# Optimization experiments

Measured on AMD Instinct MI355X. Metric: run time of the kernel, lower is better.

## Reference

```python
import jax, jax.numpy as jnp
from jax import lax
import numpy as np

N, BITS, NCLS = 2048, 64, 100
LAMBDA = 1.0
ALPHA = 1.0


def setup_inputs() -> dict:
    key = jax.random.key(0)
    ku, kl = jax.random.split(key)
    u = jax.random.normal(ku, (N, BITS), dtype=jnp.float32)
    labels = jax.random.randint(kl, (N,), 0, NCLS)
    y = jax.nn.one_hot(labels, NCLS, dtype=jnp.float32)  # [N, C]
    return {"u": u, "y": y}


def reference(u, y):
    # inner_product[i, j] = <u_i, u_j>;  s[i, j] = (y_i . y_j > 0)
    ip = u @ u.T                      # [N, N]
    s = (y @ y.T) > 0                 # [N, N] bool

    def step(carry, xs):
        tot, cnt = carry
        ip_row, s_row = xs            # [N], [N]
        pos = s_row
        neg = ~s_row
        # triple[p, n] = ip[p] - ip[n] - ALPHA, clamped like the original
        T = jnp.clip(ip_row[:, None] - ip_row[None, :] - ALPHA, -100.0, 50.0)
        # -(T - log(1 + exp(T))) = softplus(T) - T
        L = jax.nn.softplus(T) - T    # [N, N]
        pm = (pos[:, None] & neg[None, :]).astype(L.dtype)
        npairs = pm.sum()
        valid = (pos.sum() > 0) & (neg.sum() > 0)
        row_loss = jnp.where(valid, (L * pm).sum() / jnp.maximum(npairs, 1.0), 0.0)
        return (tot + row_loss, cnt + valid.astype(jnp.float32)), None

    (tot, cnt), _ = lax.scan(step, (jnp.float32(0.0), jnp.float32(0.0)), (ip, s))
    loss1 = jnp.where(cnt > 0, tot / jnp.maximum(cnt, 1.0), 0.0)
    loss2 = LAMBDA * jnp.mean((u - jnp.sign(u)) ** 2)
    return loss1 + loss2
```

## Files before the change

kernel.cpp:

```cpp
#include <hip/hip_runtime.h>
#include <hip/hip_bf16.h>
#include <math.h>

#define NROWS 2048
#define BITS  64
#define NCLS  100
#define ALPHA_C  1.0f
#define LAMBDA_C 1.0f
#define ECLAMP   1.0e9f
#define NPMAX    64
#define EPS      20

typedef __bf16 bf16x8 __attribute__((ext_vector_type(8)));
typedef float  floatx4 __attribute__((ext_vector_type(4)));


__device__ __forceinline__ float block_reduce_sum(float v, float* wsum) {
    __syncthreads();
    #pragma unroll
    for (int off = 32; off > 0; off >>= 1) v += __shfl_down(v, off);
    int tid = threadIdx.x;
    if ((tid & 63) == 0) wsum[tid >> 6] = v;
    __syncthreads();
    float r = 0.f;
    if (tid == 0) {
        #pragma unroll
        for (int w = 0; w < 4; ++w) r += wsum[w];
    }
    return r;
}

__device__ __forceinline__ float softplus_mt(float T) {
    return fmaxf(-T, 0.f) + __logf(1.f + __expf(-fabsf(T)));
}


__global__ __launch_bounds__(256) void prep_kernel(const float* __restrict__ u,
                                                   const float* __restrict__ y,
                                                   unsigned short* __restrict__ ub,
                                                   unsigned char* __restrict__ lab8,
                                                   float* __restrict__ qp,
                                                   float* __restrict__ rl,
                                                   unsigned int* __restrict__ done) {
    const int tid = threadIdx.x;
    if (blockIdx.x < 64) {
        __shared__ float wsum[4];
        const int base = blockIdx.x * 2048 + tid * 8;
        float4 v0 = *(const float4*)(u + base);
        float4 v1 = *(const float4*)(u + base + 4);
        float vv[8] = {v0.x, v0.y, v0.z, v0.w, v1.x, v1.y, v1.z, v1.w};
        unsigned short ob[8];
        float q = 0.f;
        #pragma unroll
        for (int m = 0; m < 8; ++m) {
            const float v = vv[m];
            const float sg = (v > 0.f) ? 1.f : ((v < 0.f) ? -1.f : 0.f);
            const float d = v - sg;
            q = fmaf(d, d, q);
            __hip_bfloat16 h = __float2bfloat16(v);
            ob[m] = *reinterpret_cast<unsigned short*>(&h);
        }
        *(uint4*)(ub + base) = *(const uint4*)ob;
        float t = block_reduce_sum(q, wsum);
        if (tid == 0) qp[blockIdx.x] = t;
    } else {
        const int bi = blockIdx.x - 64;
        if (bi == 0 && tid == 0) *done = 0u;
        if (tid == 0) ((float4*)rl)[bi] = make_float4(0.f, 0.f, 0.f, 0.f);
        const int row = bi * 4 + (tid >> 6);
        const int lane = tid & 63;
        const float* yr = y + (size_t)row * NCLS;
        float v0 = yr[lane];
        float v1 = (lane < NCLS - 64) ? yr[lane + 64] : 0.f;
        unsigned long long m0 = __ballot(v0 > 0.5f);
        unsigned long long m1 = __ballot(v1 > 0.5f);
        if (lane == 0) {
            int c = m0 ? (__ffsll(m0) - 1) : (m1 ? 64 + __ffsll(m1) - 1 : 0);
            lab8[row] = (unsigned char)c;
        }
    }
}

__global__ __launch_bounds__(512, 4) void fused_kernel(const float* __restrict__ u,
                                                       const unsigned short* __restrict__ ub,
                                                       const unsigned char* __restrict__ lab8,
                                                       const float* __restrict__ qp,
                                                       float* __restrict__ rl,
                                                       unsigned int* __restrict__ done,
                                                       float* __restrict__ out) {
    __shared__ unsigned char labL[NROWS];
    __shared__ float uloc[16][BITS];
    __shared__ float epT[NPMAX][EPS];
    __shared__ int   clsIdx[NROWS];
    __shared__ int   ccnt[NCLS];
    __shared__ int   cofs[NCLS];
    __shared__ int   cpos[NCLS];
    __shared__ int   np16[16];
    __shared__ float wsum[16][8];
    __shared__ float red8[8];
    __shared__ int   lastflag;

    const int tid  = threadIdx.x;
    const int wave = tid >> 6;
    const int lane = tid & 63;
    const int rsel = lane & 15;
    const int quad = lane >> 4;
    const int koff = quad * 8;
    const int i0    = (blockIdx.x >> 2) * 16;
    const int jbase = (blockIdx.x & 3) * 512;

    ((unsigned int*)labL)[tid] = ((const unsigned int*)lab8)[tid];
    ((float2*)uloc)[tid] = ((const float2*)(u + (size_t)i0 * BITS))[tid];
    if (tid < NCLS) ccnt[tid] = 0;

    uint4 a0r = *(const uint4*)(ub + (size_t)(i0 + rsel) * BITS + koff);
    uint4 a1r = *(const uint4*)(ub + (size_t)(i0 + rsel) * BITS + 32 + koff);
    uint4 b0r[4], b1r[4];
    #pragma unroll
    for (int t = 0; t < 4; ++t) {
        const int jr = jbase + (wave * 4 + t) * 16 + rsel;
        b0r[t] = *(const uint4*)(ub + (size_t)jr * BITS + koff);
        b1r[t] = *(const uint4*)(ub + (size_t)jr * BITS + 32 + koff);
    }
    __syncthreads();

    #pragma unroll
    for (int m = 0; m < 4; ++m) atomicAdd(&ccnt[labL[tid + m * 512]], 1);
    __syncthreads();
    if (tid == 0) {
        int run = 0;
        for (int c = 0; c < NCLS; ++c) { cofs[c] = run; run += ccnt[c]; }
    }
    __syncthreads();
    if (tid < NCLS) cpos[tid] = cofs[tid];
    __syncthreads();
    #pragma unroll
    for (int m = 0; m < 4; ++m) {
        const int j = tid + m * 512;
        const int p = atomicAdd(&cpos[labL[j]], 1);
        clsIdx[p] = j;
    }

    bf16x8 A0 = __builtin_bit_cast(bf16x8, a0r);
    bf16x8 A1 = __builtin_bit_cast(bf16x8, a1r);
    float Eb[4][4];
    #pragma unroll
    for (int t = 0; t < 4; ++t) {
        bf16x8 B0 = __builtin_bit_cast(bf16x8, b0r[t]);
        bf16x8 B1 = __builtin_bit_cast(bf16x8, b1r[t]);
        floatx4 cacc = {0.f, 0.f, 0.f, 0.f};
        cacc = __builtin_amdgcn_mfma_f32_16x16x32_bf16(A0, B0, cacc, 0, 0, 0);
        cacc = __builtin_amdgcn_mfma_f32_16x16x32_bf16(A1, B1, cacc, 0, 0, 0);
        const int jr = jbase + (wave * 4 + t) * 16 + rsel;
        const int colLab = labL[jr];
        #pragma unroll
        for (int r = 0; r < 4; ++r) {
            const int rowLab = labL[i0 + 4 * quad + r];
            Eb[t][r] = (colLab == rowLab) ? 0.f
                                          : fminf(__expf(cacc[r] + ALPHA_C), ECLAMP);
        }
    }
    __syncthreads();

    #pragma unroll
    for (int s2 = 0; s2 < 2; ++s2) {
        const int r16 = wave * 2 + s2;
        const int ci  = labL[i0 + r16];
        const int np  = ccnt[ci];
        const int base = cofs[ci];
        const int npc = (np < NPMAX) ? np : NPMAX;
        float val = 0.f;
        if (lane < npc) {
            const int j = clsIdx[base + lane];
            const float4* uj4 = (const float4*)(u + (size_t)j * BITS);
            const float4* ui4 = (const float4*)(&uloc[r16][0]);
            float s0 = 0.f, s1 = 0.f, s2v = 0.f, s3 = 0.f;
            #pragma unroll
            for (int kk = 0; kk < BITS / 4; ++kk) {
                float4 vj = uj4[kk];
                float4 vi = ui4[kk];
                s0 = fmaf(vj.x, vi.x, s0);
                s1 = fmaf(vj.y, vi.y, s1);
                s2v = fmaf(vj.z, vi.z, s2v);
                s3 = fmaf(vj.w, vi.w, s3);
            }
            val = fminf(__expf(-((s0 + s1) + (s2v + s3))), ECLAMP);
        }
        epT[lane][r16] = val;
        if (lane == 0) np16[r16] = np;
    }
    __syncthreads();

    int npmx = 0;
    #pragma unroll
    for (int r = 0; r < 16; ++r) {
        int n = np16[r]; n = (n > NPMAX) ? NPMAX : n;
        npmx = (n > npmx) ? n : npmx;
    }
    const int npr = (npmx + 1) & ~1;

    float s[4] = {0.f, 0.f, 0.f, 0.f};
    for (int k = 0; k < npr; k += 2) {
        const float4 e0 = *(const float4*)(&epT[k][4 * quad]);
        const float4 e1 = *(const float4*)(&epT[k + 1][4 * quad]);
        const float e0v[4] = {e0.x, e0.y, e0.z, e0.w};
        const float e1v[4] = {e1.x, e1.y, e1.z, e1.w};
        #pragma unroll
        for (int t = 0; t < 4; ++t) {
            #pragma unroll
            for (int r = 0; r < 4; ++r) {
                const float q0 = Eb[t][r];
                const float f = fmaf(q0, e0v[r], 1.f);
                const float g = fmaf(q0, e1v[r], 1.f);
                s[r] += __log2f(f * g);
            }
        }
    }

    #pragma unroll
    for (int r = 0; r < 4; ++r) {
        #pragma unroll
        for (int off = 1; off < 16; off <<= 1) s[r] += __shfl_xor(s[r], off);
    }
    if (rsel == 0) {
        #pragma unroll
        for (int r = 0; r < 4; ++r) wsum[4 * quad + r][wave] = s[r];
    }
    __syncthreads();
    if (tid < 16) {
        const float ln2 = 0.6931471805599453f;
        const float tot = (((wsum[tid][0] + wsum[tid][1]) +
                            (wsum[tid][2] + wsum[tid][3])) +
                           ((wsum[tid][4] + wsum[tid][5]) +
                            (wsum[tid][6] + wsum[tid][7]))) * ln2;
        atomicAdd(&rl[i0 + tid], tot);
    }
    __syncthreads();

    if (tid == 0) {
        __threadfence();
        const unsigned int old = atomicAdd(done, 1u);
        lastflag = (old == 511u) ? 1 : 0;
    }
    __syncthreads();
    if (lastflag) {
        float tsum = 0.f, vsum = 0.f;
        for (int row = tid; row < NROWS; row += 512) {
            const float rv = atomicAdd(&rl[row], 0.0f);
            const int np = ccnt[labL[row]];
            const int nn = NROWS - np;
            const int valid = (np > 0 && nn > 0) ? 1 : 0;
            tsum += valid ? (rv / fmaxf((float)np * (float)nn, 1.f)) : 0.f;
            vsum += (float)valid;
        }
        float q = (tid < 64) ? qp[tid] : 0.f;

        float vals[3] = {tsum, vsum, q};
        float outv[3];
        #pragma unroll
        for (int m = 0; m < 3; ++m) {
            float v = vals[m];
            #pragma unroll
            for (int off = 32; off > 0; off >>= 1) v += __shfl_down(v, off);
            if (lane == 0) red8[wave] = v;
            __syncthreads();
            float r = 0.f;
            if (tid == 0) {
                #pragma unroll
                for (int w = 0; w < 8; ++w) r += red8[w];
            }
            __syncthreads();
            outv[m] = r;
        }
        if (tid == 0) {
            const float loss1 = (outv[1] > 0.f) ? (outv[0] / fmaxf(outv[1], 1.f)) : 0.f;
            const float loss2 = LAMBDA_C * (outv[2] / (float)(NROWS * BITS));
            out[0] = loss1 + loss2;
        }
    }
}


__global__ __launch_bounds__(256) void labels_only_kernel(const float* __restrict__ y,
                                                          int* __restrict__ labels) {
    const int tid = threadIdx.x;
    const int row = blockIdx.x * 4 + (tid >> 6);
    const int lane = tid & 63;
    const float* yr = y + (size_t)row * NCLS;
    float v0 = yr[lane];
    float v1 = (lane < NCLS - 64) ? yr[lane + 64] : 0.f;
    unsigned long long m0 = __ballot(v0 > 0.5f);
    unsigned long long m1 = __ballot(v1 > 0.5f);
    if (lane == 0) {
        int c = m0 ? (__ffsll(m0) - 1) : (m1 ? 64 + __ffsll(m1) - 1 : 0);
        labels[row] = c;
    }
}

__global__ __launch_bounds__(256) void row_loss_kernel(const float* __restrict__ u,
                                                       const int* __restrict__ labels,
                                                       float* __restrict__ acc) {
    __shared__ float a[NROWS];
    __shared__ float apv[NROWS];
    __shared__ int lab[NROWS];
    __shared__ float ui[BITS];
    __shared__ int npos_s;
    __shared__ float wsum[4];

    const int i = blockIdx.x;
    const int tid = threadIdx.x;

    if (tid < BITS) ui[tid] = u[(size_t)i * BITS + tid];
    if (tid == 0) npos_s = 0;
    __syncthreads();

    #pragma unroll
    for (int m = 0; m < NROWS / 256; ++m) {
        const int j = tid + m * 256;
        const float4* uj = (const float4*)(u + (size_t)j * BITS);
        float s0 = 0.f, s1 = 0.f, s2 = 0.f, s3 = 0.f;
        #pragma unroll
        for (int q = 0; q < BITS / 4; ++q) {
            float4 v = uj[q];
            s0 = fmaf(v.x, ui[4 * q + 0], s0);
            s1 = fmaf(v.y, ui[4 * q + 1], s1);
            s2 = fmaf(v.z, ui[4 * q + 2], s2);
            s3 = fmaf(v.w, ui[4 * q + 3], s3);
        }
        a[j] = (s0 + s1) + (s2 + s3);
        lab[j] = labels[j];
    }
    __syncthreads();

    const int c = lab[i];
    #pragma unroll
    for (int m = 0; m < NROWS / 256; ++m) {
        const int j = tid + m * 256;
        if (lab[j] == c) { int k = atomicAdd(&npos_s, 1); apv[k] = a[j]; }
    }
    __syncthreads();
    const int npos = npos_s;
    const int nneg = NROWS - npos;

    float b[NROWS / 256];
    #pragma unroll
    for (int m = 0; m < NROWS / 256; ++m) {
        const int j = tid + m * 256;
        b[m] = (lab[j] != c) ? (a[j] + ALPHA_C) : -3.0e38f;
    }

    float lsum = 0.f;
    for (int k = 0; k < npos; ++k) {
        const float apk = apv[k];
        #pragma unroll
        for (int m = 0; m < NROWS / 256; ++m) lsum += softplus_mt(apk - b[m]);
    }

    float tot = block_reduce_sum(lsum, wsum);
    if (tid == 0) {
        const int valid = (npos > 0 && nneg > 0) ? 1 : 0;
        const float npairs = fmaxf((float)npos * (float)nneg, 1.f);
        const float rlv = valid ? (tot / npairs) : 0.f;
        atomicAdd(&acc[0], rlv);
        atomicAdd(&acc[1], (float)valid);
    }
}

__global__ __launch_bounds__(256) void quant_kernel(const float* __restrict__ u,
                                                    float* __restrict__ acc) {
    __shared__ float wsum[4];
    const int stride = gridDim.x * 256;
    float s = 0.f;
    for (int t = blockIdx.x * 256 + threadIdx.x; t < NROWS * BITS; t += stride) {
        float v = u[t];
        float sg = (v > 0.f) ? 1.f : ((v < 0.f) ? -1.f : 0.f);
        float d = v - sg;
        s = fmaf(d, d, s);
    }
    float tot = block_reduce_sum(s, wsum);
    if (threadIdx.x == 0) atomicAdd(&acc[2], tot);
}

__global__ void finalize_kernel(const float* __restrict__ acc,
                                float* __restrict__ out) {
    const float tot = acc[0], cnt = acc[1], q = acc[2];
    const float loss1 = (cnt > 0.f) ? (tot / fmaxf(cnt, 1.f)) : 0.f;
    const float loss2 = LAMBDA_C * (q / (float)(NROWS * BITS));
    out[0] = loss1 + loss2;
}


extern "C" void kernel_launch(void* const* d_in, const int* in_sizes, int n_in,
                              void* d_out, int out_size, void* d_ws, size_t ws_size,
                              hipStream_t stream) {
    const float* u = (const float*)d_in[0];
    const float* y = (const float*)d_in[1];
    float* out = (float*)d_out;

    unsigned char* lab8 = (unsigned char*)d_ws;
    unsigned int* done = (unsigned int*)((char*)d_ws + 4096);
    float* rl = (float*)((char*)d_ws + 8192);
    float* qp = (float*)((char*)d_ws + 16384);
    unsigned short* ub = (unsigned short*)((char*)d_ws + 24576);
    const size_t NEED = 24576 + (size_t)NROWS * BITS * sizeof(unsigned short);

    if (ws_size >= NEED) {
        prep_kernel<<<576, 256, 0, stream>>>(u, y, ub, lab8, qp, rl, done);
        fused_kernel<<<512, 512, 0, stream>>>(u, ub, lab8, qp, rl, done, out);
    } else {
        float* acc2 = (float*)d_ws;
        int*   lab2 = (int*)((char*)d_ws + 256);
        hipMemsetAsync(d_ws, 0, 256, stream);
        labels_only_kernel<<<512, 256, 0, stream>>>(y, lab2);
        row_loss_kernel<<<NROWS, 256, 0, stream>>>(u, lab2, acc2);
        quant_kernel<<<64, 256, 0, stream>>>(u, acc2);
        finalize_kernel<<<1, 1, 0, stream>>>(acc2, out);
    }
}
```

Baseline: 84.46 us.

## Replace per-pair log2 with exponent/mantissa product accumulation and defer MFMA

The hot pair-sum loop used to call log2 on each product of two softplus factors. It now multiplies four factors at a time, with two of them pre-scaled by 2^-60 so the product cannot overflow. It adds the raw exponent bits to an integer accumulator and multiplies the mantissas into a running product, so only one log2 per output row is needed at the end. The bf16 B-tile loads and the MFMA/exp block move to after the class-bucketing and positive-term stage, which shortens the live range of those registers. The exclusive-scan pass and the cpos copy are also merged, removing one barrier. The exponent trick adds integer and bit work, and its correctness depends on the scaling keeping every partial product in normal float range.

```diff
diff --git a/kernel.cpp b/kernel.cpp
--- a/kernel.cpp
+++ b/kernel.cpp
@@ -115,13 +115,6 @@
 
     uint4 a0r = *(const uint4*)(ub + (size_t)(i0 + rsel) * BITS + koff);
     uint4 a1r = *(const uint4*)(ub + (size_t)(i0 + rsel) * BITS + 32 + koff);
-    uint4 b0r[4], b1r[4];
-    #pragma unroll
-    for (int t = 0; t < 4; ++t) {
-        const int jr = jbase + (wave * 4 + t) * 16 + rsel;
-        b0r[t] = *(const uint4*)(ub + (size_t)jr * BITS + koff);
-        b1r[t] = *(const uint4*)(ub + (size_t)jr * BITS + 32 + koff);
-    }
     __syncthreads();
 
     #pragma unroll
@@ -129,36 +122,14 @@
     __syncthreads();
     if (tid == 0) {
         int run = 0;
-        for (int c = 0; c < NCLS; ++c) { cofs[c] = run; run += ccnt[c]; }
-    }
-    __syncthreads();
-    if (tid < NCLS) cpos[tid] = cofs[tid];
+        for (int c = 0; c < NCLS; ++c) { cofs[c] = run; cpos[c] = run; run += ccnt[c]; }
+    }
     __syncthreads();
     #pragma unroll
     for (int m = 0; m < 4; ++m) {
         const int j = tid + m * 512;
         const int p = atomicAdd(&cpos[labL[j]], 1);
         clsIdx[p] = j;
-    }
-
-    bf16x8 A0 = __builtin_bit_cast(bf16x8, a0r);
-    bf16x8 A1 = __builtin_bit_cast(bf16x8, a1r);
-    float Eb[4][4];
-    #pragma unroll
-    for (int t = 0; t < 4; ++t) {
-        bf16x8 B0 = __builtin_bit_cast(bf16x8, b0r[t]);
-        bf16x8 B1 = __builtin_bit_cast(bf16x8, b1r[t]);
-        floatx4 cacc = {0.f, 0.f, 0.f, 0.f};
-        cacc = __builtin_amdgcn_mfma_f32_16x16x32_bf16(A0, B0, cacc, 0, 0, 0);
-        cacc = __builtin_amdgcn_mfma_f32_16x16x32_bf16(A1, B1, cacc, 0, 0, 0);
-        const int jr = jbase + (wave * 4 + t) * 16 + rsel;
-        const int colLab = labL[jr];
-        #pragma unroll
-        for (int r = 0; r < 4; ++r) {
-            const int rowLab = labL[i0 + 4 * quad + r];
-            Eb[t][r] = (colLab == rowLab) ? 0.f
-                                          : fminf(__expf(cacc[r] + ALPHA_C), ECLAMP);
-        }
     }
     __syncthreads();
 
@@ -191,31 +162,71 @@
     }
     __syncthreads();
 
+    const bf16x8 A0 = __builtin_bit_cast(bf16x8, a0r);
+    const bf16x8 A1 = __builtin_bit_cast(bf16x8, a1r);
+    float Eb[4][4];
+    #pragma unroll
+    for (int t = 0; t < 4; ++t) {
+        const int jr = jbase + (wave * 4 + t) * 16 + rsel;
+        uint4 b0r = *(const uint4*)(ub + (size_t)jr * BITS + koff);
+        uint4 b1r = *(const uint4*)(ub + (size_t)jr * BITS + 32 + koff);
+        bf16x8 B0 = __builtin_bit_cast(bf16x8, b0r);
+        bf16x8 B1 = __builtin_bit_cast(bf16x8, b1r);
+        floatx4 cacc = {0.f, 0.f, 0.f, 0.f};
+        cacc = __builtin_amdgcn_mfma_f32_16x16x32_bf16(A0, B0, cacc, 0, 0, 0);
+        cacc = __builtin_amdgcn_mfma_f32_16x16x32_bf16(A1, B1, cacc, 0, 0, 0);
+        const int colLab = labL[jr];
+        #pragma unroll
+        for (int r = 0; r < 4; ++r) {
+            const int rowLab = labL[i0 + 4 * quad + r];
+            Eb[t][r] = (colLab == rowLab) ? 0.f
+                                          : fminf(__expf(cacc[r] + ALPHA_C), ECLAMP);
+        }
+    }
+
     int npmx = 0;
     #pragma unroll
     for (int r = 0; r < 16; ++r) {
         int n = np16[r]; n = (n > NPMAX) ? NPMAX : n;
         npmx = (n > npmx) ? n : npmx;
     }
-    const int npr = (npmx + 1) & ~1;
-
-    float s[4] = {0.f, 0.f, 0.f, 0.f};
-    for (int k = 0; k < npr; k += 2) {
+    const int npr4 = (npmx + 3) & ~3;
+
+    const float SC = 0x1p-60f;
+    float mprod[4] = {1.f, 1.f, 1.f, 1.f};
+    int   eacc[4]  = {0, 0, 0, 0};
+    for (int k = 0; k < npr4; k += 4) {
         const float4 e0 = *(const float4*)(&epT[k][4 * quad]);
         const float4 e1 = *(const float4*)(&epT[k + 1][4 * quad]);
-        const float e0v[4] = {e0.x, e0.y, e0.z, e0.w};
+        const float4 e2 = *(const float4*)(&epT[k + 2][4 * quad]);
+        const float4 e3 = *(const float4*)(&epT[k + 3][4 * quad]);
+        const float e0c[4] = {e0.x * SC, e0.y * SC, e0.z * SC, e0.w * SC};
         const float e1v[4] = {e1.x, e1.y, e1.z, e1.w};
+        const float e2c[4] = {e2.x * SC, e2.y * SC, e2.z * SC, e2.w * SC};
+        const float e3v[4] = {e3.x, e3.y, e3.z, e3.w};
         #pragma unroll
         for (int t = 0; t < 4; ++t) {
             #pragma unroll
             for (int r = 0; r < 4; ++r) {
                 const float q0 = Eb[t][r];
-                const float f = fmaf(q0, e0v[r], 1.f);
-                const float g = fmaf(q0, e1v[r], 1.f);
-                s[r] += __log2f(f * g);
+                const float f0 = fmaf(q0, e0c[r], SC);
+                const float f1 = fmaf(q0, e1v[r], 1.f);
+                const float f2 = fmaf(q0, e2c[r], SC);
+                const float f3 = fmaf(q0, e3v[r], 1.f);
+                const float P  = (f0 * f1) * (f2 * f3);
+                const unsigned int pb = __builtin_bit_cast(unsigned int, P);
+                eacc[r] += (int)(pb >> 23);
+                const float m = __builtin_bit_cast(float,
+                                    (pb & 0x007FFFFFu) | 0x3F800000u);
+                mprod[r] *= m;
             }
         }
     }
+    const float nadj = 7.0f * (float)npr4;
+    float s[4];
+    #pragma unroll
+    for (int r = 0; r < 4; ++r)
+        s[r] = ((float)eacc[r] - nadj) + __log2f(mprod[r]);
 
     #pragma unroll
     for (int r = 0; r < 4; ++r) {
```

Result: faster. 81.98 us (-2.9%).
